# Kernel tuning notes

Measured on AMD Instinct MI355X. Metric: run time of the kernel, lower is better.

## Reference

```python
import jax, jax.numpy as jnp
import numpy as np

PST_THD = 0.05
NMS_THD = 0.5
TOP_K = 1000  # max candidates kept before greedy NMS (fixed for jit)
IMG = 1024
NUM_CLASSES = 80


def _make_anchors(H, W):
    # Standard RetinaNet anchors: P3-P7, 3 ratios x 3 scales = 9 per location.
    levels = [3, 4, 5, 6, 7]
    ratios = np.array([0.5, 1.0, 2.0])
    scales = np.array([2 ** 0, 2 ** (1.0 / 3.0), 2 ** (2.0 / 3.0)])
    all_a = []
    for l in levels:
        stride = 2 ** l
        size = 2 ** (l + 2)
        base = []
        for r in ratios:
            for s in scales:
                area = (size * s) ** 2
                w = np.sqrt(area / r)
                h = w * r
                base.append([-w / 2, -h / 2, w / 2, h / 2])
        base = np.asarray(base)  # (9,4)
        fh, fw = H // stride, W // stride
        sx = (np.arange(fw) + 0.5) * stride
        sy = (np.arange(fh) + 0.5) * stride
        sxx, syy = np.meshgrid(sx, sy)
        shifts = np.stack([sxx.ravel(), syy.ravel(), sxx.ravel(), syy.ravel()], 1)
        all_a.append((shifts[:, None, :] + base[None, :, :]).reshape(-1, 4))
    return np.concatenate(all_a, 0).astype(np.float32)  # (A,4)


def setup_inputs() -> dict:
    key = jax.random.key(0)
    k1, k2 = jax.random.split(key)
    anchors = jnp.asarray(_make_anchors(IMG, IMG))  # (A,4)
    A = anchors.shape[0]
    classification = jax.random.uniform(k1, (1, A, NUM_CLASSES), dtype=jnp.float32)
    regression = jax.random.normal(k2, (1, A, 4), dtype=jnp.float32) * 0.5
    return {
        "classification": classification,
        "regression": regression,
        "anchors": anchors,
        "height": IMG,
        "width": IMG,
    }


def _postprocess(classification, regression, anchors, height, width):
    cls = classification[0]   # (A,C)
    reg = regression[0]       # (A,4)
    # --- BBoxTransform (std = [0.1,0.1,0.2,0.2]) ---
    wa = anchors[:, 2] - anchors[:, 0]
    ha = anchors[:, 3] - anchors[:, 1]
    cxa = anchors[:, 0] + 0.5 * wa
    cya = anchors[:, 1] + 0.5 * ha
    pcx = cxa + reg[:, 0] * 0.1 * wa
    pcy = cya + reg[:, 1] * 0.1 * ha
    pw = jnp.exp(reg[:, 2] * 0.2) * wa
    ph = jnp.exp(reg[:, 3] * 0.2) * ha
    # --- ClipBoxes ---
    x1 = jnp.clip(pcx - 0.5 * pw, 0.0, None)
    y1 = jnp.clip(pcy - 0.5 * ph, 0.0, None)
    x2 = jnp.minimum(pcx + 0.5 * pw, jnp.float32(width))
    y2 = jnp.minimum(pcy + 0.5 * ph, jnp.float32(height))
    boxes = jnp.stack([x1, y1, x2, y2], axis=1)  # (A,4)
    # --- score threshold + top-K candidate selection ---
    scores = jnp.max(cls, axis=1)
    class_id = jnp.argmax(cls, axis=1).astype(jnp.int32)
    masked = jnp.where(scores > PST_THD, scores, -1.0)
    top_s, idx = jax.lax.top_k(masked, TOP_K)  # sorted descending
    b = boxes[idx]                             # (K,4)
    c = class_id[idx]
    valid = top_s > PST_THD
    # --- greedy NMS over K candidates (classic py_cpu_nms, +1 areas) ---
    area = (b[:, 2] - b[:, 0] + 1.0) * (b[:, 3] - b[:, 1] + 1.0)
    xx1 = jnp.maximum(b[:, None, 0], b[None, :, 0])
    yy1 = jnp.maximum(b[:, None, 1], b[None, :, 1])
    xx2 = jnp.minimum(b[:, None, 2], b[None, :, 2])
    yy2 = jnp.minimum(b[:, None, 3], b[None, :, 3])
    inter = jnp.clip(xx2 - xx1 + 1.0, 0.0) * jnp.clip(yy2 - yy1 + 1.0, 0.0)
    iou = inter / (area[:, None] + area[None, :] - inter)  # (K,K)
    later = jnp.arange(TOP_K)

    def body(i, keep):
        supp = (iou[i] > NMS_THD) & (later > i) & keep[i]
        return keep & (~supp)

    keep = jax.lax.fori_loop(0, TOP_K, body, valid)
    nms_scores = jnp.where(keep, top_s, 0.0)
    nms_classes = jnp.where(keep, c, -1)
    nms_boxes = jnp.where(keep[:, None], b, 0.0)
    return nms_scores, nms_classes, nms_boxes


def reference(classification, regression, anchors, height, width):
    # Fixed-size padded equivalent of the original variable-length NMS output.
    return _postprocess(classification, regression, anchors, height, width)
```

## Files before the change

kernel.cpp:

```cpp
#include <hip/hip_runtime.h>
#include <stdint.h>

#define K_TOP 1000
#define PST 0.05f
#define THR 256
#define NTAIL 64

#define C_DONE0 0
#define C_BAR   4
#define C_CNTA  6
#define C_CNTE  7
#define C_PREFIX 8
#define C_CUM    9

typedef unsigned long long ull;

__device__ __forceinline__ unsigned mapU(float f) {
  unsigned b = __float_as_uint(f);
  return (b & 0x80000000u) ? ~b : (b | 0x80000000u);
}
__device__ __forceinline__ float unmapU(unsigned u) {
  unsigned b = (u & 0x80000000u) ? (u ^ 0x80000000u) : ~u;
  return __uint_as_float(b);
}
__device__ __forceinline__ float scalar_dim(const int* p) {
  int v = *p;
  if (v > 0 && v < (1 << 20)) return (float)v;
  return __int_as_float(v);
}

template <int NB>
__device__ void selectN(const unsigned* __restrict__ histL, int shift,
                        unsigned* __restrict__ ctrl) {
  constexpr int PB = NB / 64;
  int t = threadIdx.x;
  unsigned cumIn = ctrl[C_CUM];
  unsigned need = (unsigned)K_TOP - cumIn;
  unsigned h[PB];
  unsigned v = 0;
  #pragma unroll
  for (int b = 0; b < PB; ++b) { h[b] = histL[PB * t + b]; v += h[b]; }
  #pragma unroll
  for (int d = 1; d < 64; d <<= 1) {
    unsigned q = __shfl_down(v, d);
    if (t + d < 64) v += q;
  }
  unsigned sn = __shfl_down(v, 1);
  if (t == 63) sn = 0;
  if (v >= need && sn < need) {
    unsigned c = sn;
    int bsel = PB * t;
    for (int b = PB - 1; b >= 0; --b) {
      if (c + h[b] >= need) { bsel = PB * t + b; break; }
      c += h[b];
    }
    ctrl[C_PREFIX] = ctrl[C_PREFIX] | (((unsigned)bsel) << shift);
    ctrl[C_CUM] = cumIn + c;
  }
}

template <int NB>
__device__ void selectL(const unsigned* __restrict__ histL, int shift,
                        unsigned* sPref, unsigned* sCum) {
  constexpr int PB = NB / 64;
  int t = threadIdx.x;
  unsigned cumIn = *sCum;
  unsigned need = (unsigned)K_TOP - cumIn;
  unsigned h[PB];
  unsigned v = 0;
  #pragma unroll
  for (int b = 0; b < PB; ++b) { h[b] = histL[PB * t + b]; v += h[b]; }
  #pragma unroll
  for (int d = 1; d < 64; d <<= 1) {
    unsigned q = __shfl_down(v, d);
    if (t + d < 64) v += q;
  }
  unsigned sn = __shfl_down(v, 1);
  if (t == 63) sn = 0;
  if (v >= need && sn < need) {
    unsigned c = sn;
    int bsel = PB * t;
    for (int b = PB - 1; b >= 0; --b) {
      if (c + h[b] >= need) { bsel = PB * t + b; break; }
      c += h[b];
    }
    *sPref = *sPref | (((unsigned)bsel) << shift);
    *sCum = cumIn + c;
  }
}

__device__ __forceinline__ void gsync(unsigned* bar, unsigned target) {
  __syncthreads();
  if (threadIdx.x == 0) {
    __hip_atomic_fetch_add(bar, 1u, __ATOMIC_ACQ_REL, __HIP_MEMORY_SCOPE_AGENT);
    while (__hip_atomic_load(bar, __ATOMIC_RELAXED, __HIP_MEMORY_SCOPE_AGENT) < target)
      __builtin_amdgcn_s_sleep(1);
    (void)__hip_atomic_load(bar, __ATOMIC_ACQUIRE, __HIP_MEMORY_SCOPE_AGENT);
  }
  __syncthreads();
}

__global__ void __launch_bounds__(1024) k_init(unsigned* hist, unsigned* ctrl,
                                               ull* keyBuf, float* candS,
                                               int* candC, float4* candB) {
  int t = threadIdx.x;
  for (int e = t; e < 5120; e += 1024) hist[e] = 0u;
  if (t < 64) ctrl[t] = 0u;
  for (int e = t; e < 4096; e += 1024) keyBuf[e] = 0ull;
  candS[t] = -1.0f;
  candC[t] = -1;
  candB[t] = make_float4(0.f, 0.f, 0.f, 0.f);
}

__global__ void __launch_bounds__(THR) k_decode(
    const float* __restrict__ cls, const float* __restrict__ reg,
    const float* __restrict__ anc, const int* __restrict__ hp,
    const int* __restrict__ wp, int A, int C, int pairMode,
    float4* __restrict__ boxes, unsigned* __restrict__ su,
    int* __restrict__ ci, unsigned* hist0, unsigned* ctrl, int nb) {
  __shared__ unsigned lh[2048];
  int t = threadIdx.x;
  for (int b = t; b < 2048; b += THR) lh[b] = 0u;
  __syncthreads();
  float W = scalar_dim(wp), H = scalar_dim(hp);

  if (pairMode) {
    int g = blockIdx.x * THR + t;
    if (g < 2 * A) {
      int a = g >> 1, hh = g & 1;
      const float4* rp = (const float4*)(cls + (size_t)a * 80 + hh * 40);
      float4 v[10];
      #pragma unroll
      for (int j = 0; j < 10; ++j) v[j] = rp[j];
      float mx[10];
      #pragma unroll
      for (int j = 0; j < 10; ++j)
        mx[j] = fmaxf(fmaxf(v[j].x, v[j].y), fmaxf(v[j].z, v[j].w));
      float m = mx[0];
      #pragma unroll
      for (int j = 1; j < 10; ++j) m = fmaxf(m, mx[j]);
      int mi = 0x7fffffff;
      #pragma unroll
      for (int j = 0; j < 10; ++j) {
        mi = min(mi, (v[j].x == m) ? 4 * j + 0 : 0x7fffffff);
        mi = min(mi, (v[j].y == m) ? 4 * j + 1 : 0x7fffffff);
        mi = min(mi, (v[j].z == m) ? 4 * j + 2 : 0x7fffffff);
        mi = min(mi, (v[j].w == m) ? 4 * j + 3 : 0x7fffffff);
      }
      mi += hh * 40;
      float mo = __shfl_xor(m, 1);
      int mio = __shfl_xor(mi, 1);
      if (mo > m) { m = mo; mi = mio; }
      if (hh == 0) {
        float4 an = ((const float4*)anc)[a];
        float4 rg = ((const float4*)reg)[a];
        float wa = an.z - an.x, ha = an.w - an.y;
        float cxa = an.x + 0.5f * wa, cya = an.y + 0.5f * ha;
        float pcx = cxa + rg.x * 0.1f * wa;
        float pcy = cya + rg.y * 0.1f * ha;
        float pw = expf(rg.z * 0.2f) * wa;
        float ph = expf(rg.w * 0.2f) * ha;
        float x1 = fmaxf(pcx - 0.5f * pw, 0.f);
        float y1 = fmaxf(pcy - 0.5f * ph, 0.f);
        float x2 = fminf(pcx + 0.5f * pw, W);
        float y2 = fminf(pcy + 0.5f * ph, H);
        boxes[a] = make_float4(x1, y1, x2, y2);
        ci[a] = mi;
        float msk = (m > PST) ? m : -1.0f;
        unsigned u = mapU(msk);
        su[a] = u;
        atomicAdd(&lh[u >> 21], 1u);
      }
    }
  } else {
    int a = blockIdx.x * THR + t;
    if (a < A) {
      const float* row = cls + (size_t)a * C;
      float m = -3.4e38f; int mi = 0;
      for (int j = 0; j < C; ++j) { float v = row[j]; if (v > m) { m = v; mi = j; } }
      float4 an = ((const float4*)anc)[a];
      float4 rg = ((const float4*)reg)[a];
      float wa = an.z - an.x, ha = an.w - an.y;
      float cxa = an.x + 0.5f * wa, cya = an.y + 0.5f * ha;
      float pcx = cxa + rg.x * 0.1f * wa;
      float pcy = cya + rg.y * 0.1f * ha;
      float pw = expf(rg.z * 0.2f) * wa;
      float ph = expf(rg.w * 0.2f) * ha;
      float x1 = fmaxf(pcx - 0.5f * pw, 0.f);
      float y1 = fmaxf(pcy - 0.5f * ph, 0.f);
      float x2 = fminf(pcx + 0.5f * pw, W);
      float y2 = fminf(pcy + 0.5f * ph, H);
      boxes[a] = make_float4(x1, y1, x2, y2);
      ci[a] = mi;
      float msk = (m > PST) ? m : -1.0f;
      unsigned u = mapU(msk);
      su[a] = u;
      atomicAdd(&lh[u >> 21], 1u);
    }
  }
  __syncthreads();
  for (int b = t; b < 2048; b += THR)
    if (lh[b]) atomicAdd(&hist0[b], lh[b]);
  __shared__ int last;
  __syncthreads();
  if (t == 0) {
    unsigned old = __hip_atomic_fetch_add(&ctrl[C_DONE0], 1u,
                                          __ATOMIC_ACQ_REL, __HIP_MEMORY_SCOPE_AGENT);
    last = (old == (unsigned)(nb - 1));
  }
  __syncthreads();
  if (last && t < 64) selectN<2048>(hist0, 21, ctrl);
}

__global__ void __launch_bounds__(THR) k_tail(
    const unsigned* __restrict__ su, int A,
    const float4* __restrict__ boxes, const int* __restrict__ ci,
    ull* __restrict__ keyBuf, float* __restrict__ candS,
    int* __restrict__ candC, float4* __restrict__ candB,
    ull* __restrict__ maskBuf, unsigned* hist, unsigned* ctrl,
    float* __restrict__ out) {
  __shared__ ull shmem[2048];
  __shared__ ull keepW[16];
  __shared__ unsigned lh[2048];
  __shared__ unsigned sPref, sCum;
  int t = threadIdx.x;
  int g0 = blockIdx.x * THR + t;

  if (t == 0) { sPref = ctrl[C_PREFIX]; sCum = ctrl[C_CUM]; }

  for (int b = t; b < 2048; b += THR) lh[b] = 0u;
  __syncthreads();
  unsigned pref = sPref;
  for (int a = g0; a < A; a += NTAIL * THR) {
    unsigned u = su[a];
    if ((u & 0xFFE00000u) == pref) atomicAdd(&lh[(u >> 10) & 2047u], 1u);
  }
  __syncthreads();
  for (int b = t; b < 2048; b += THR)
    if (lh[b]) atomicAdd(&hist[2048 + b], lh[b]);
  gsync(&ctrl[C_BAR], NTAIL);
  if (t < 64) selectL<2048>(hist + 2048, 10, &sPref, &sCum);
  __syncthreads();

  for (int b = t; b < 1024; b += THR) lh[b] = 0u;
  __syncthreads();
  pref = sPref;
  for (int a = g0; a < A; a += NTAIL * THR) {
    unsigned u = su[a];
    if ((u & 0xFFFFFC00u) == pref) atomicAdd(&lh[u & 1023u], 1u);
  }
  __syncthreads();
  for (int b = t; b < 1024; b += THR)
    if (lh[b]) atomicAdd(&hist[4096 + b], lh[b]);
  gsync(&ctrl[C_BAR], 2 * NTAIL);
  if (t < 64) selectL<1024>(hist + 4096, 0, &sPref, &sCum);
  __syncthreads();
  unsigned uT = sPref;

  for (int a = g0; a < A; a += NTAIL * THR) {
    unsigned u = su[a];
    if (u > uT) {
      unsigned p = atomicAdd(&ctrl[C_CNTA], 1u);
      if (p < 1000u) keyBuf[p] = (((ull)u) << 32) | (unsigned)(~a);
    } else if (u == uT) {
      unsigned p = atomicAdd(&ctrl[C_CNTE], 1u);
      if (p < 3072u) keyBuf[1024 + p] = (((ull)u) << 32) | (unsigned)(~a);
    }
  }
  gsync(&ctrl[C_BAR], 3 * NTAIL);

  unsigned nTop = ctrl[C_CNTA];
  unsigned nTie = ctrl[C_CNTE]; if (nTie > 3072u) nTie = 3072u;
  for (int e = t; e < 1024; e += THR) shmem[e] = keyBuf[e];
  __syncthreads();
  int wid = t >> 6, lane = t & 63;
  int gw = blockIdx.x * 4 + wid;
  #pragma unroll
  for (int s2 = 0; s2 < 4; ++s2) {
    int sidx = gw * 4 + s2;
    ull k0 = shmem[sidx];
    if (k0 != 0ull) {
      unsigned cnt = 0;
      for (int e = lane; e < 1024; e += 64) cnt += (shmem[e] > k0) ? 1u : 0u;
      #pragma unroll
      for (int d = 32; d; d >>= 1) cnt += __shfl_down(cnt, d);
      if (lane == 0 && cnt < (unsigned)K_TOP) {
        unsigned idx = ~(unsigned)k0;
        candS[cnt] = unmapU((unsigned)(k0 >> 32));
        candC[cnt] = ci[idx];
        candB[cnt] = boxes[idx];
      }
    }
  }
  for (int tix = gw; tix < (int)nTie; tix += NTAIL * 4) {
    ull k0 = keyBuf[1024 + tix];
    unsigned cnt = 0;
    for (int e = lane; e < (int)nTie; e += 64) cnt += (keyBuf[1024 + e] > k0) ? 1u : 0u;
    #pragma unroll
    for (int d = 32; d; d >>= 1) cnt += __shfl_down(cnt, d);
    if (lane == 0) {
      unsigned rank = nTop + cnt;
      if (rank < (unsigned)K_TOP) {
        unsigned idx = ~(unsigned)k0;
        candS[rank] = unmapU((unsigned)(k0 >> 32));
        candC[rank] = ci[idx];
        candB[rank] = boxes[idx];
      }
    }
  }
  gsync(&ctrl[C_BAR], 4 * NTAIL);

  float4* sCand = (float4*)shmem;
  for (int e = t; e < 1024; e += THR) sCand[e] = candB[e];
  __syncthreads();
  {
    int g4 = blockIdx.x * THR + t;
    int i = g4 & 1023, w = g4 >> 10;
    float4 bi = sCand[i];
    float areai = (bi.z - bi.x + 1.f) * (bi.w - bi.y + 1.f);
    ull bits = 0ull;
    if (i < K_TOP) {
      int j0 = w << 6;
      #pragma unroll 4
      for (int b = 0; b < 64; ++b) {
        int j = j0 + b;
        if (j > i && j < K_TOP) {
          float4 bj = sCand[j];
          float xx1 = fmaxf(bi.x, bj.x);
          float yy1 = fmaxf(bi.y, bj.y);
          float xx2 = fminf(bi.z, bj.z);
          float yy2 = fminf(bi.w, bj.w);
          float iw = fmaxf(xx2 - xx1 + 1.f, 0.f);
          float ih = fmaxf(yy2 - yy1 + 1.f, 0.f);
          float inter = iw * ih;
          float areaj = (bj.z - bj.x + 1.f) * (bj.w - bj.y + 1.f);
          float iou = inter / (areai + areaj - inter);
          if (iou > 0.5f) bits |= (1ull << b);
        }
      }
    }
    maskBuf[i * 16 + w] = bits;
  }
  gsync(&ctrl[C_BAR], 5 * NTAIL);

  if (blockIdx.x != 0) return;
  ull (*buf)[1024] = (ull(*)[1024])shmem;
  __syncthreads();
  for (int e = t; e < 1024; e += THR) buf[0][e] = maskBuf[e];
  __syncthreads();

  unsigned long long remv = 0ull;
  int l = t & 63;
  if (t < 64 && l < 16) {
    ull vb = 0ull;
    for (int b = 0; b < 64; ++b) {
      float s = candS[(l << 6) + b];
      if (s > PST) vb |= (1ull << b);
    }
    remv = ~vb;
  }
  for (int w = 0; w < 16; ++w) {
    if (w + 1 < 16 && t >= 64) {
      for (int e = t - 64; e < 1024; e += THR - 64)
        buf[(w + 1) & 1][e] = maskBuf[(w + 1) * 1024 + e];
    }
    if (t < 64) {
      ull cw = __shfl(remv, w);
      const ull* rows = buf[w & 1];
      #pragma unroll
      for (int b = 0; b < 64; ++b) {
        ull mrow = rows[b * 16 + (l & 15)];
        ull mvw  = rows[b * 16 + w];
        ull sel = ((cw >> b) & 1ull) - 1ull;
        remv |= (mrow & sel);
        cw   |= (mvw & sel);
      }
    }
    __syncthreads();
  }
  if (t < 64 && l < 16) keepW[l] = ~remv;
  __syncthreads();

  for (int q = t; q < K_TOP; q += THR) {
    bool kp = (keepW[q >> 6] >> (q & 63)) & 1ull;
    float sc = candS[q];
    int cc = candC[q];
    float4 bb = candB[q];
    out[q] = kp ? sc : 0.f;
    out[K_TOP + q] = kp ? (float)cc : -1.f;
    float4 ob = kp ? bb : make_float4(0.f, 0.f, 0.f, 0.f);
    *(float4*)(out + 2 * K_TOP + 4 * q) = ob;
  }
}

extern "C" void kernel_launch(void* const* d_in, const int* in_sizes, int n_in,
                              void* d_out, int out_size, void* d_ws, size_t ws_size,
                              hipStream_t stream) {
  const float* cls = (const float*)d_in[0];
  const float* reg = (const float*)d_in[1];
  const float* anc = (const float*)d_in[2];
  const int* hp = (const int*)d_in[3];
  const int* wp = (const int*)d_in[4];
  int A = in_sizes[2] / 4;
  int C = in_sizes[0] / A;

  char* ws = (char*)d_ws;
  size_t off = 0;
  auto alloc = [&](size_t bytes) -> void* {
    void* p = ws + off;
    off = (off + bytes + 255) & ~(size_t)255;
    return p;
  };
  float4* boxes = (float4*)alloc((size_t)A * 16);
  unsigned* su = (unsigned*)alloc((size_t)A * 4);
  int* ci = (int*)alloc((size_t)A * 4);
  ull* keyBuf = (ull*)alloc(4096 * 8);
  float* candS = (float*)alloc(1024 * 4);
  int* candC = (int*)alloc(1024 * 4);
  float4* candB = (float4*)alloc(1024 * 16);
  ull* maskBuf = (ull*)alloc(16384 * 8);
  unsigned* hist = (unsigned*)alloc(5120 * 4);
  unsigned* ctrl = (unsigned*)alloc(256 * 4);
  (void)ws_size; (void)n_in; (void)out_size;

  int pairMode = (C == 80) ? 1 : 0;
  int nb1 = pairMode ? (2 * A + THR - 1) / THR : (A + THR - 1) / THR;

  hipLaunchKernelGGL(k_init, dim3(1), dim3(1024), 0, stream,
                     hist, ctrl, keyBuf, candS, candC, candB);
  hipLaunchKernelGGL(k_decode, dim3(nb1), dim3(THR), 0, stream,
                     cls, reg, anc, hp, wp, A, C, pairMode,
                     boxes, su, ci, hist, ctrl, nb1);
  hipLaunchKernelGGL(k_tail, dim3(NTAIL), dim3(THR), 0, stream,
                     su, A, boxes, ci, keyBuf, candS, candC, candB,
                     maskBuf, hist, ctrl, (float*)d_out);
}
```

Before: 248.8 us.

## Stage class scores through padded LDS tiles and relax grid-barrier memory ordering

The decode kernel now cooperatively loads 128 rows of class scores into padded shared memory with coalesced float4 reads, then one thread per row scans the row for its argmax, replacing the two-threads-per-row register approach. Separately, the grid barrier drops its acquire/release ordering, and the cross-block buffers are read and written with relaxed agent-scope atomic loads and stores so data stays coherent without heavy fences. This targets global load efficiency in decode and barrier overhead in the tail. Only half the threads do the argmax, and the relaxed barrier relies on those atomics for correctness.

```diff
diff --git a/kernel.cpp b/kernel.cpp
--- a/kernel.cpp
+++ b/kernel.cpp
@@ -5,6 +5,8 @@
 #define PST 0.05f
 #define THR 256
 #define NTAIL 64
+#define ROWS 128
+#define PADW 81
 
 #define C_DONE0 0
 #define C_BAR   4
@@ -27,6 +29,29 @@
   int v = *p;
   if (v > 0 && v < (1 << 20)) return (float)v;
   return __int_as_float(v);
+}
+
+__device__ __forceinline__ unsigned aldU(const unsigned* p) {
+  return __hip_atomic_load(p, __ATOMIC_RELAXED, __HIP_MEMORY_SCOPE_AGENT);
+}
+__device__ __forceinline__ void astU(unsigned* p, unsigned v) {
+  __hip_atomic_store(p, v, __ATOMIC_RELAXED, __HIP_MEMORY_SCOPE_AGENT);
+}
+__device__ __forceinline__ ull aldL(const ull* p) {
+  return __hip_atomic_load(p, __ATOMIC_RELAXED, __HIP_MEMORY_SCOPE_AGENT);
+}
+__device__ __forceinline__ void astL(ull* p, ull v) {
+  __hip_atomic_store(p, v, __ATOMIC_RELAXED, __HIP_MEMORY_SCOPE_AGENT);
+}
+
+__device__ __forceinline__ void gsync(unsigned* bar, unsigned target) {
+  __syncthreads();
+  if (threadIdx.x == 0) {
+    __hip_atomic_fetch_add(bar, 1u, __ATOMIC_RELAXED, __HIP_MEMORY_SCOPE_AGENT);
+    while (__hip_atomic_load(bar, __ATOMIC_RELAXED, __HIP_MEMORY_SCOPE_AGENT) < target)
+      __builtin_amdgcn_s_sleep(1);
+  }
+  __syncthreads();
 }
 
 template <int NB>
@@ -69,7 +94,7 @@
   unsigned h[PB];
   unsigned v = 0;
   #pragma unroll
-  for (int b = 0; b < PB; ++b) { h[b] = histL[PB * t + b]; v += h[b]; }
+  for (int b = 0; b < PB; ++b) { h[b] = aldU(&histL[PB * t + b]); v += h[b]; }
   #pragma unroll
   for (int d = 1; d < 64; d <<= 1) {
     unsigned q = __shfl_down(v, d);
@@ -89,15 +114,22 @@
   }
 }
 
-__device__ __forceinline__ void gsync(unsigned* bar, unsigned target) {
-  __syncthreads();
-  if (threadIdx.x == 0) {
-    __hip_atomic_fetch_add(bar, 1u, __ATOMIC_ACQ_REL, __HIP_MEMORY_SCOPE_AGENT);
-    while (__hip_atomic_load(bar, __ATOMIC_RELAXED, __HIP_MEMORY_SCOPE_AGENT) < target)
-      __builtin_amdgcn_s_sleep(1);
-    (void)__hip_atomic_load(bar, __ATOMIC_ACQUIRE, __HIP_MEMORY_SCOPE_AGENT);
-  }
-  __syncthreads();
+__device__ __forceinline__ void decode_box(int a, const float4* anc4,
+                                           const float4* reg4, float W, float H,
+                                           float4* boxes) {
+  float4 an = anc4[a];
+  float4 rg = reg4[a];
+  float wa = an.z - an.x, ha = an.w - an.y;
+  float cxa = an.x + 0.5f * wa, cya = an.y + 0.5f * ha;
+  float pcx = cxa + rg.x * 0.1f * wa;
+  float pcy = cya + rg.y * 0.1f * ha;
+  float pw = expf(rg.z * 0.2f) * wa;
+  float ph = expf(rg.w * 0.2f) * ha;
+  float x1 = fmaxf(pcx - 0.5f * pw, 0.f);
+  float y1 = fmaxf(pcy - 0.5f * ph, 0.f);
+  float x2 = fminf(pcx + 0.5f * pw, W);
+  float y2 = fminf(pcy + 0.5f * ph, H);
+  boxes[a] = make_float4(x1, y1, x2, y2);
 }
 
 __global__ void __launch_bounds__(1024) k_init(unsigned* hist, unsigned* ctrl,
@@ -112,91 +144,86 @@
   candB[t] = make_float4(0.f, 0.f, 0.f, 0.f);
 }
 
-__global__ void __launch_bounds__(THR) k_decode(
+__global__ void __launch_bounds__(THR) k_decode_staged(
     const float* __restrict__ cls, const float* __restrict__ reg,
     const float* __restrict__ anc, const int* __restrict__ hp,
-    const int* __restrict__ wp, int A, int C, int pairMode,
+    const int* __restrict__ wp, int A,
     float4* __restrict__ boxes, unsigned* __restrict__ su,
     int* __restrict__ ci, unsigned* hist0, unsigned* ctrl, int nb) {
+  __shared__ float s[ROWS * PADW];
   __shared__ unsigned lh[2048];
   int t = threadIdx.x;
+  int r0 = blockIdx.x * ROWS;
   for (int b = t; b < 2048; b += THR) lh[b] = 0u;
-  __syncthreads();
-  float W = scalar_dim(wp), H = scalar_dim(hp);
-
-  if (pairMode) {
-    int g = blockIdx.x * THR + t;
-    if (g < 2 * A) {
-      int a = g >> 1, hh = g & 1;
-      const float4* rp = (const float4*)(cls + (size_t)a * 80 + hh * 40);
-      float4 v[10];
+
+  const float4* g4 = (const float4*)cls;
+  #pragma unroll
+  for (int i = 0; i < 10; ++i) {
+    int f = t + THR * i;
+    int row = f / 20, c4 = f % 20;
+    if (r0 + row < A) {
+      float4 v = g4[(size_t)r0 * 20 + f];
+      int base = row * PADW + c4 * 4;
+      s[base + 0] = v.x; s[base + 1] = v.y; s[base + 2] = v.z; s[base + 3] = v.w;
+    }
+  }
+  __syncthreads();
+
+  if (t < ROWS) {
+    int a = r0 + t;
+    if (a < A) {
+      const float* rowp = s + t * PADW;
+      float m = rowp[0]; int mi = 0;
       #pragma unroll
-      for (int j = 0; j < 10; ++j) v[j] = rp[j];
-      float mx[10];
-      #pragma unroll
-      for (int j = 0; j < 10; ++j)
-        mx[j] = fmaxf(fmaxf(v[j].x, v[j].y), fmaxf(v[j].z, v[j].w));
-      float m = mx[0];
-      #pragma unroll
-      for (int j = 1; j < 10; ++j) m = fmaxf(m, mx[j]);
-      int mi = 0x7fffffff;
-      #pragma unroll
-      for (int j = 0; j < 10; ++j) {
-        mi = min(mi, (v[j].x == m) ? 4 * j + 0 : 0x7fffffff);
-        mi = min(mi, (v[j].y == m) ? 4 * j + 1 : 0x7fffffff);
-        mi = min(mi, (v[j].z == m) ? 4 * j + 2 : 0x7fffffff);
-        mi = min(mi, (v[j].w == m) ? 4 * j + 3 : 0x7fffffff);
+      for (int j = 1; j < 80; ++j) {
+        float v = rowp[j];
+        if (v > m) { m = v; mi = j; }
       }
-      mi += hh * 40;
-      float mo = __shfl_xor(m, 1);
-      int mio = __shfl_xor(mi, 1);
-      if (mo > m) { m = mo; mi = mio; }
-      if (hh == 0) {
-        float4 an = ((const float4*)anc)[a];
-        float4 rg = ((const float4*)reg)[a];
-        float wa = an.z - an.x, ha = an.w - an.y;
-        float cxa = an.x + 0.5f * wa, cya = an.y + 0.5f * ha;
-        float pcx = cxa + rg.x * 0.1f * wa;
-        float pcy = cya + rg.y * 0.1f * ha;
-        float pw = expf(rg.z * 0.2f) * wa;
-        float ph = expf(rg.w * 0.2f) * ha;
-        float x1 = fmaxf(pcx - 0.5f * pw, 0.f);
-        float y1 = fmaxf(pcy - 0.5f * ph, 0.f);
-        float x2 = fminf(pcx + 0.5f * pw, W);
-        float y2 = fminf(pcy + 0.5f * ph, H);
-        boxes[a] = make_float4(x1, y1, x2, y2);
-        ci[a] = mi;
-        float msk = (m > PST) ? m : -1.0f;
-        unsigned u = mapU(msk);
-        su[a] = u;
-        atomicAdd(&lh[u >> 21], 1u);
-      }
-    }
-  } else {
-    int a = blockIdx.x * THR + t;
-    if (a < A) {
-      const float* row = cls + (size_t)a * C;
-      float m = -3.4e38f; int mi = 0;
-      for (int j = 0; j < C; ++j) { float v = row[j]; if (v > m) { m = v; mi = j; } }
-      float4 an = ((const float4*)anc)[a];
-      float4 rg = ((const float4*)reg)[a];
-      float wa = an.z - an.x, ha = an.w - an.y;
-      float cxa = an.x + 0.5f * wa, cya = an.y + 0.5f * ha;
-      float pcx = cxa + rg.x * 0.1f * wa;
-      float pcy = cya + rg.y * 0.1f * ha;
-      float pw = expf(rg.z * 0.2f) * wa;
-      float ph = expf(rg.w * 0.2f) * ha;
-      float x1 = fmaxf(pcx - 0.5f * pw, 0.f);
-      float y1 = fmaxf(pcy - 0.5f * ph, 0.f);
-      float x2 = fminf(pcx + 0.5f * pw, W);
-      float y2 = fminf(pcy + 0.5f * ph, H);
-      boxes[a] = make_float4(x1, y1, x2, y2);
+      float W = scalar_dim(wp), H = scalar_dim(hp);
+      decode_box(a, (const float4*)anc, (const float4*)reg, W, H, boxes);
       ci[a] = mi;
       float msk = (m > PST) ? m : -1.0f;
       unsigned u = mapU(msk);
       su[a] = u;
       atomicAdd(&lh[u >> 21], 1u);
     }
+  }
+  __syncthreads();
+  for (int b = t; b < 2048; b += THR)
+    if (lh[b]) atomicAdd(&hist0[b], lh[b]);
+  __shared__ int last;
+  __syncthreads();
+  if (t == 0) {
+    unsigned old = __hip_atomic_fetch_add(&ctrl[C_DONE0], 1u,
+                                          __ATOMIC_ACQ_REL, __HIP_MEMORY_SCOPE_AGENT);
+    last = (old == (unsigned)(nb - 1));
+  }
+  __syncthreads();
+  if (last && t < 64) selectN<2048>(hist0, 21, ctrl);
+}
+
+__global__ void __launch_bounds__(THR) k_decode_generic(
+    const float* __restrict__ cls, const float* __restrict__ reg,
+    const float* __restrict__ anc, const int* __restrict__ hp,
+    const int* __restrict__ wp, int A, int C,
+    float4* __restrict__ boxes, unsigned* __restrict__ su,
+    int* __restrict__ ci, unsigned* hist0, unsigned* ctrl, int nb) {
+  __shared__ unsigned lh[2048];
+  int t = threadIdx.x;
+  for (int b = t; b < 2048; b += THR) lh[b] = 0u;
+  __syncthreads();
+  int a = blockIdx.x * THR + t;
+  if (a < A) {
+    const float* row = cls + (size_t)a * C;
+    float m = -3.4e38f; int mi = 0;
+    for (int j = 0; j < C; ++j) { float v = row[j]; if (v > m) { m = v; mi = j; } }
+    float W = scalar_dim(wp), H = scalar_dim(hp);
+    decode_box(a, (const float4*)anc, (const float4*)reg, W, H, boxes);
+    ci[a] = mi;
+    float msk = (m > PST) ? m : -1.0f;
+    unsigned u = mapU(msk);
+    su[a] = u;
+    atomicAdd(&lh[u >> 21], 1u);
   }
   __syncthreads();
   for (int b = t; b < 2048; b += THR)
@@ -261,17 +288,17 @@
     unsigned u = su[a];
     if (u > uT) {
       unsigned p = atomicAdd(&ctrl[C_CNTA], 1u);
-      if (p < 1000u) keyBuf[p] = (((ull)u) << 32) | (unsigned)(~a);
+      if (p < 1000u) astL(&keyBuf[p], (((ull)u) << 32) | (unsigned)(~a));
     } else if (u == uT) {
       unsigned p = atomicAdd(&ctrl[C_CNTE], 1u);
-      if (p < 3072u) keyBuf[1024 + p] = (((ull)u) << 32) | (unsigned)(~a);
+      if (p < 3072u) astL(&keyBuf[1024 + p], (((ull)u) << 32) | (unsigned)(~a));
     }
   }
   gsync(&ctrl[C_BAR], 3 * NTAIL);
 
-  unsigned nTop = ctrl[C_CNTA];
-  unsigned nTie = ctrl[C_CNTE]; if (nTie > 3072u) nTie = 3072u;
-  for (int e = t; e < 1024; e += THR) shmem[e] = keyBuf[e];
+  unsigned nTop = aldU(&ctrl[C_CNTA]);
+  unsigned nTie = aldU(&ctrl[C_CNTE]); if (nTie > 3072u) nTie = 3072u;
+  for (int e = t; e < 1024; e += THR) shmem[e] = aldL(&keyBuf[e]);
   __syncthreads();
   int wid = t >> 6, lane = t & 63;
   int gw = blockIdx.x * 4 + wid;
@@ -286,32 +313,46 @@
       for (int d = 32; d; d >>= 1) cnt += __shfl_down(cnt, d);
       if (lane == 0 && cnt < (unsigned)K_TOP) {
         unsigned idx = ~(unsigned)k0;
-        candS[cnt] = unmapU((unsigned)(k0 >> 32));
-        candC[cnt] = ci[idx];
-        candB[cnt] = boxes[idx];
+        float4 bb = boxes[idx];
+        astU((unsigned*)&candS[cnt], __float_as_uint(unmapU((unsigned)(k0 >> 32))));
+        astU((unsigned*)&candC[cnt], (unsigned)ci[idx]);
+        ull* bp = (ull*)&candB[cnt];
+        astL(bp, ((ull)__float_as_uint(bb.y) << 32) | __float_as_uint(bb.x));
+        astL(bp + 1, ((ull)__float_as_uint(bb.w) << 32) | __float_as_uint(bb.z));
       }
     }
   }
   for (int tix = gw; tix < (int)nTie; tix += NTAIL * 4) {
-    ull k0 = keyBuf[1024 + tix];
+    ull k0 = aldL(&keyBuf[1024 + tix]);
     unsigned cnt = 0;
-    for (int e = lane; e < (int)nTie; e += 64) cnt += (keyBuf[1024 + e] > k0) ? 1u : 0u;
+    for (int e = lane; e < (int)nTie; e += 64)
+      cnt += (aldL(&keyBuf[1024 + e]) > k0) ? 1u : 0u;
     #pragma unroll
     for (int d = 32; d; d >>= 1) cnt += __shfl_down(cnt, d);
     if (lane == 0) {
       unsigned rank = nTop + cnt;
       if (rank < (unsigned)K_TOP) {
         unsigned idx = ~(unsigned)k0;
-        candS[rank] = unmapU((unsigned)(k0 >> 32));
-        candC[rank] = ci[idx];
-        candB[rank] = boxes[idx];
+        float4 bb = boxes[idx];
+        astU((unsigned*)&candS[rank], __float_as_uint(unmapU((unsigned)(k0 >> 32))));
+        astU((unsigned*)&candC[rank], (unsigned)ci[idx]);
+        ull* bp = (ull*)&candB[rank];
+        astL(bp, ((ull)__float_as_uint(bb.y) << 32) | __float_as_uint(bb.x));
+        astL(bp + 1, ((ull)__float_as_uint(bb.w) << 32) | __float_as_uint(bb.z));
       }
     }
   }
   gsync(&ctrl[C_BAR], 4 * NTAIL);
 
   float4* sCand = (float4*)shmem;
-  for (int e = t; e < 1024; e += THR) sCand[e] = candB[e];
+  for (int e = t; e < 1024; e += THR) {
+    const ull* bp = (const ull*)&candB[e];
+    ull lo = aldL(bp), hi = aldL(bp + 1);
+    sCand[e] = make_float4(__uint_as_float((unsigned)lo),
+                           __uint_as_float((unsigned)(lo >> 32)),
+                           __uint_as_float((unsigned)hi),
+                           __uint_as_float((unsigned)(hi >> 32)));
+  }
   __syncthreads();
   {
     int g4 = blockIdx.x * THR + t;
@@ -339,14 +380,14 @@
         }
       }
     }
-    maskBuf[i * 16 + w] = bits;
+    astL(&maskBuf[i * 16 + w], bits);
   }
   gsync(&ctrl[C_BAR], 5 * NTAIL);
 
   if (blockIdx.x != 0) return;
   ull (*buf)[1024] = (ull(*)[1024])shmem;
   __syncthreads();
-  for (int e = t; e < 1024; e += THR) buf[0][e] = maskBuf[e];
+  for (int e = t; e < 1024; e += THR) buf[0][e] = aldL(&maskBuf[e]);
   __syncthreads();
 
   unsigned long long remv = 0ull;
@@ -354,7 +395,7 @@
   if (t < 64 && l < 16) {
     ull vb = 0ull;
     for (int b = 0; b < 64; ++b) {
-      float s = candS[(l << 6) + b];
+      float s = __uint_as_float(aldU((const unsigned*)&candS[(l << 6) + b]));
       if (s > PST) vb |= (1ull << b);
     }
     remv = ~vb;
@@ -362,7 +403,7 @@
   for (int w = 0; w < 16; ++w) {
     if (w + 1 < 16 && t >= 64) {
       for (int e = t - 64; e < 1024; e += THR - 64)
-        buf[(w + 1) & 1][e] = maskBuf[(w + 1) * 1024 + e];
+        buf[(w + 1) & 1][e] = aldL(&maskBuf[(w + 1) * 1024 + e]);
     }
     if (t < 64) {
       ull cw = __shfl(remv, w);
@@ -383,12 +424,17 @@
 
   for (int q = t; q < K_TOP; q += THR) {
     bool kp = (keepW[q >> 6] >> (q & 63)) & 1ull;
-    float sc = candS[q];
-    int cc = candC[q];
-    float4 bb = candB[q];
+    float sc = __uint_as_float(aldU((const unsigned*)&candS[q]));
+    int cc = (int)aldU((const unsigned*)&candC[q]);
+    const ull* bp = (const ull*)&candB[q];
+    ull lo = aldL(bp), hi = aldL(bp + 1);
     out[q] = kp ? sc : 0.f;
     out[K_TOP + q] = kp ? (float)cc : -1.f;
-    float4 ob = kp ? bb : make_float4(0.f, 0.f, 0.f, 0.f);
+    float4 ob = kp ? make_float4(__uint_as_float((unsigned)lo),
+                                 __uint_as_float((unsigned)(lo >> 32)),
+                                 __uint_as_float((unsigned)hi),
+                                 __uint_as_float((unsigned)(hi >> 32)))
+                   : make_float4(0.f, 0.f, 0.f, 0.f);
     *(float4*)(out + 2 * K_TOP + 4 * q) = ob;
   }
 }
@@ -423,14 +469,19 @@
   unsigned* ctrl = (unsigned*)alloc(256 * 4);
   (void)ws_size; (void)n_in; (void)out_size;
 
-  int pairMode = (C == 80) ? 1 : 0;
-  int nb1 = pairMode ? (2 * A + THR - 1) / THR : (A + THR - 1) / THR;
-
   hipLaunchKernelGGL(k_init, dim3(1), dim3(1024), 0, stream,
                      hist, ctrl, keyBuf, candS, candC, candB);
-  hipLaunchKernelGGL(k_decode, dim3(nb1), dim3(THR), 0, stream,
-                     cls, reg, anc, hp, wp, A, C, pairMode,
-                     boxes, su, ci, hist, ctrl, nb1);
+  if (C == 80) {
+    int nb = (A + ROWS - 1) / ROWS;
+    hipLaunchKernelGGL(k_decode_staged, dim3(nb), dim3(THR), 0, stream,
+                       cls, reg, anc, hp, wp, A,
+                       boxes, su, ci, hist, ctrl, nb);
+  } else {
+    int nb = (A + THR - 1) / THR;
+    hipLaunchKernelGGL(k_decode_generic, dim3(nb), dim3(THR), 0, stream,
+                       cls, reg, anc, hp, wp, A, C,
+                       boxes, su, ci, hist, ctrl, nb);
+  }
   hipLaunchKernelGGL(k_tail, dim3(NTAIL), dim3(THR), 0, stream,
                      su, A, boxes, ci, keyBuf, candS, candC, candB,
                      maskBuf, hist, ctrl, (float*)d_out);
```

Result: faster. 228.4 us (-8.2%).
